# Performance work log

Measured on AMD Instinct MI355X. Metric: run time of the kernel, lower is better.

## Reference

```python
import jax, jax.numpy as jnp
import numpy as np

N_HEAD = 16
MA_K = 0.02          # sigmoid temperature in ma_k_activation
LEAKY_SLOPE = 0.02   # negative_slope in ma_q_activation
NEG_INF = -1e9


def setup_inputs() -> dict:
    key = jax.random.key(0)
    k1, k2, k3, k4 = jax.random.split(key, 4)
    B, T, C = 2, 2048, 1024
    x = jax.random.normal(k1, (B, T, C), dtype=jnp.float32)
    s = 1.0 / np.sqrt(C)
    W_attn = jax.random.normal(k2, (C, 2 * C), dtype=jnp.float32) * s
    W_k2 = jax.random.normal(k3, (C, C), dtype=jnp.float32) * s
    W_proj = jax.random.normal(k4, (C, C), dtype=jnp.float32) * s
    return {"x": x, "W_attn": W_attn, "W_k2": W_k2, "W_proj": W_proj}


def _heads(t, H):
    # [B,T,C] -> [B,H,T,d]
    B, T, C = t.shape
    return t.reshape(B, T, H, C // H).transpose(0, 2, 1, 3)


def reference(x, W_attn, W_k2, W_proj):
    B, T, C = x.shape
    H = N_HEAD
    d = C // H
    scale = 1.0 / jnp.sqrt(jnp.asarray(d, x.dtype))

    qk = x @ W_attn                      # [B,T,2C]
    q, k = jnp.split(qk, 2, axis=-1)
    q = _heads(q, H)                     # [B,H,T,d]
    k = _heads(k, H)
    v = _heads(x, H)                     # v = x

    # --- AR branch: causal softmax attention ---
    scores = jnp.einsum('bhtd,bhsd->bhts', q, k) * scale
    causal = jnp.tril(jnp.ones((T, T), dtype=bool))
    scores = jnp.where(causal, scores, NEG_INF)
    attn = jax.nn.softmax(scores, axis=-1)
    y = jnp.einsum('bhts,bhsd->bhtd', attn, v)   # [B,H,T,d]

    # --- MA branch: causal, softmax-free linear attention on residual ---
    e = v[:, :, 1:, :] - y[:, :, :-1, :]          # [B,H,T-1,d]
    k2 = _heads(x[:, :-1, :] @ W_k2, H)           # [B,H,T-1,d]
    q2 = q[:, :, 1:, :]                           # [B,H,T-1,d]

    qa = -jax.nn.leaky_relu(-q2 * scale, negative_slope=LEAKY_SLOPE)
    ka = jax.nn.sigmoid(MA_K * (k2 * scale))

    w = jnp.einsum('bhtd,bhsd->bhts', qa, ka)     # [B,H,T-1,T-1]
    w = jnp.tril(w)
    y2 = jnp.einsum('bhts,bhsd->bhtd', w, e)      # [B,H,T-1,d]
    y2 = jnp.concatenate([jnp.zeros_like(y2[:, :, :1, :]), y2], axis=2)  # pad front

    def merge(t):  # [B,H,T,d] -> [B,T,C]
        return t.transpose(0, 2, 1, 3).reshape(B, T, C)

    return merge(y) @ W_proj + merge(y2) @ W_proj
```

## Files before the change

kernel.cpp:

```cpp
#include <hip/hip_runtime.h>

typedef unsigned short u16;
typedef u16   u16x4  __attribute__((ext_vector_type(4)));
typedef u16   u16x8  __attribute__((ext_vector_type(8)));
typedef __bf16 bf16x8 __attribute__((ext_vector_type(8)));
typedef float  f32x4  __attribute__((ext_vector_type(4)));

__device__ __forceinline__ float bf2f(u16 v) {
    unsigned u = ((unsigned)v) << 16;
    return __builtin_bit_cast(float, u);
}
__device__ __forceinline__ u16 f2bf(float f) {
    unsigned u = __builtin_bit_cast(unsigned, f);
    u += 0x7fffu + ((u >> 16) & 1u);
    return (u16)(u >> 16);
}

__device__ __forceinline__ size_t kimg_idx(int bh, int s, int d) {
    return ((size_t)(bh * 32 + (s >> 6)) * 4096) + (size_t)(((d >> 3) * 64 + (s & 63)) * 8) + (d & 7);
}
__device__ __forceinline__ size_t vimg_idx(int bh, int s, int d) {
    return ((size_t)(bh * 32 + (s >> 6)) * 4096) + (size_t)((((s & 63) >> 3) * 64 + d) * 8) + (s & 7);
}

__global__ __launch_bounds__(256)
void convert_pack(const float* __restrict__ in, u16* __restrict__ xb,
                  u16* __restrict__ xpack) {
    int i = blockIdx.x * 256 + threadIdx.x;
    int c4 = i & 255, row = i >> 8;
    int s = row & 2047, b = row >> 11;
    float4 v = ((const float4*)in)[i];
    u16x4 o;
    o.x = f2bf(v.x); o.y = f2bf(v.y); o.z = f2bf(v.z); o.w = f2bf(v.w);
    ((u16x4*)xb)[i] = o;
    int h = c4 >> 4, d0 = (c4 & 15) * 4;
    size_t base = vimg_idx(b * 16 + h, s, d0);
    xpack[base]      = o.x;
    xpack[base + 8]  = o.y;
    xpack[base + 16] = o.z;
    xpack[base + 24] = o.w;
}

__global__ __launch_bounds__(256)
void prep_weights(const float* __restrict__ Wa, const float* __restrict__ Wk,
                  const float* __restrict__ Wp, u16* __restrict__ Wta,
                  u16* __restrict__ Wtk, u16* __restrict__ Wtp) {
    __shared__ u16 tile[64][65];
    const int bx = blockIdx.x;
    const float* in; u16* out; int Cd, cx;
    if (bx < 32)      { in = Wa; out = Wta; Cd = 2048; cx = bx; }
    else if (bx < 48) { in = Wk; out = Wtk; Cd = 1024; cx = bx - 32; }
    else              { in = Wp; out = Wtp; Cd = 1024; cx = bx - 48; }
    const int c0 = cx * 64, r0 = blockIdx.y * 64;
    const int tid = threadIdx.x;
#pragma unroll
    for (int i = 0; i < 16; ++i) {
        int idx = tid + i * 256;
        int r = idx >> 6, c = idx & 63;
        tile[r][c] = f2bf(in[(size_t)(r0 + r) * Cd + c0 + c]);
    }
    __syncthreads();
#pragma unroll
    for (int i = 0; i < 16; ++i) {
        int idx = tid + i * 256;
        int r = idx >> 6, c = idx & 63;
        out[(size_t)(c0 + r) * 1024 + r0 + c] = tile[c][r];
    }
}

__global__ __launch_bounds__(256, 2)
void gemm_qk(const u16* __restrict__ A, const u16* __restrict__ Bt,
             u16* __restrict__ qs, u16* __restrict__ kpack, int K) {
    __shared__ __align__(16) u16 As[4][128][8];
    __shared__ __align__(16) u16 Bs[4][128][8];
    const int tid = threadIdx.x;
    const int wave = tid >> 6, lane = tid & 63;
    const int m0 = blockIdx.y * 128, n0 = blockIdx.x * 128;
    const int wm = (wave >> 1) * 64, wn = (wave & 1) * 64;
    const int q = lane >> 4, mr = lane & 15;
    const int sr = tid >> 2, c8 = tid & 3;
    const u16* Ap = A + (size_t)(m0 + sr) * K + c8 * 8;
    const u16* Bp = Bt + (size_t)(n0 + sr) * K + c8 * 8;

    f32x4 acc[4][4];
#pragma unroll
    for (int i = 0; i < 4; ++i)
#pragma unroll
        for (int j = 0; j < 4; ++j) acc[i][j] = f32x4{0.f, 0.f, 0.f, 0.f};

    u16x8 a0, a1, b0, b1;
    auto gload = [&](int k0) {
        a0 = *(const u16x8*)(Ap + k0);
        a1 = *(const u16x8*)(Ap + k0 + (size_t)64 * K);
        b0 = *(const u16x8*)(Bp + k0);
        b1 = *(const u16x8*)(Bp + k0 + (size_t)64 * K);
    };
    gload(0);
    for (int k0 = 0; k0 < K; k0 += 32) {
        __syncthreads();
        *(u16x8*)&As[c8][sr][0]      = a0;
        *(u16x8*)&As[c8][sr + 64][0] = a1;
        *(u16x8*)&Bs[c8][sr][0]      = b0;
        *(u16x8*)&Bs[c8][sr + 64][0] = b1;
        __syncthreads();
        if (k0 + 32 < K) gload(k0 + 32);
        bf16x8 af[4], bfr[4];
#pragma unroll
        for (int i = 0; i < 4; ++i) af[i]  = *(const bf16x8*)&As[q][wm + i * 16 + mr][0];
#pragma unroll
        for (int j = 0; j < 4; ++j) bfr[j] = *(const bf16x8*)&Bs[q][wn + j * 16 + mr][0];
#pragma unroll
        for (int i = 0; i < 4; ++i)
#pragma unroll
            for (int j = 0; j < 4; ++j)
                acc[i][j] = __builtin_amdgcn_mfma_f32_16x16x32_bf16(af[i], bfr[j], acc[i][j], 0, 0, 0);
    }
#pragma unroll
    for (int i = 0; i < 4; ++i)
#pragma unroll
        for (int j = 0; j < 4; ++j)
#pragma unroll
            for (int r = 0; r < 4; ++r) {
                int m = m0 + wm + i * 16 + q * 4 + r;
                int n = n0 + wn + j * 16 + mr;
                float v = acc[i][j][r];
                if (n < 1024) {
                    qs[(size_t)m * 1024 + n] = f2bf(v * 0.125f);
                } else {
                    int b = m >> 11, s = m & 2047, nn = n - 1024;
                    kpack[kimg_idx(b * 16 + (nn >> 6), s, nn & 63)] = f2bf(v);
                }
            }
}

template <int EPI>
__global__ __launch_bounds__(256, 2)
void gemm64(const u16* __restrict__ A, const u16* __restrict__ Bt,
            void* __restrict__ Cv, int N, int K) {
    __shared__ __align__(16) u16 As[4][64][8];
    __shared__ __align__(16) u16 Bs[4][128][8];
    const int tid = threadIdx.x;
    const int wave = tid >> 6, lane = tid & 63;
    const int m0 = blockIdx.y * 64, n0 = blockIdx.x * 128;
    const int wn0 = wave * 32;
    const int q = lane >> 4, mr = lane & 15;
    const int sr = tid >> 2, c8 = tid & 3;
    const u16* Ap = A + (size_t)(m0 + sr) * K + c8 * 8;
    const u16* Bp = Bt + (size_t)(n0 + sr) * K + c8 * 8;

    f32x4 acc[4][2];
#pragma unroll
    for (int i = 0; i < 4; ++i)
#pragma unroll
        for (int j = 0; j < 2; ++j) acc[i][j] = f32x4{0.f, 0.f, 0.f, 0.f};

    u16x8 a0, b0, b1;
    auto gload = [&](int k0) {
        a0 = *(const u16x8*)(Ap + k0);
        b0 = *(const u16x8*)(Bp + k0);
        b1 = *(const u16x8*)(Bp + k0 + (size_t)64 * K);
    };
    gload(0);
    for (int k0 = 0; k0 < K; k0 += 32) {
        __syncthreads();
        *(u16x8*)&As[c8][sr][0]      = a0;
        *(u16x8*)&Bs[c8][sr][0]      = b0;
        *(u16x8*)&Bs[c8][sr + 64][0] = b1;
        __syncthreads();
        if (k0 + 32 < K) gload(k0 + 32);
        bf16x8 af[4], bfr[2];
#pragma unroll
        for (int i = 0; i < 4; ++i) af[i]  = *(const bf16x8*)&As[q][i * 16 + mr][0];
#pragma unroll
        for (int j = 0; j < 2; ++j) bfr[j] = *(const bf16x8*)&Bs[q][wn0 + j * 16 + mr][0];
#pragma unroll
        for (int i = 0; i < 4; ++i)
#pragma unroll
            for (int j = 0; j < 2; ++j)
                acc[i][j] = __builtin_amdgcn_mfma_f32_16x16x32_bf16(af[i], bfr[j], acc[i][j], 0, 0, 0);
    }
#pragma unroll
    for (int i = 0; i < 4; ++i)
#pragma unroll
        for (int j = 0; j < 2; ++j)
#pragma unroll
            for (int r = 0; r < 4; ++r) {
                int m = m0 + i * 16 + q * 4 + r;
                int n = n0 + wn0 + j * 16 + mr;
                float v = acc[i][j][r];
                if (EPI == 1) {
                    ((float*)Cv)[(size_t)m * N + n] = v;
                } else {
                    int b = m >> 11, s = m & 2047;
                    ((u16*)Cv)[kimg_idx(b * 16 + (n >> 6), s, n & 63)] =
                        f2bf(1.f / (1.f + __expf(-0.0025f * v)));
                }
            }
}

__global__ __launch_bounds__(256, 2)
void flash_mfma(const u16* __restrict__ qs, const u16* __restrict__ kpack,
                const u16* __restrict__ xpack, u16* __restrict__ Opart,
                float* __restrict__ lpart) {
    __shared__ __align__(16) u16 Ks[8][64][8];
    __shared__ __align__(16) u16 Vs[8][64][8];
    __shared__ __align__(16) u16 Ps[4][16][72];
    const int bh = blockIdx.y, b = bh >> 4, hc = (bh & 15) * 64;
    const int z = blockIdx.z;
    const int tid = threadIdx.x, w = tid >> 6, lane = tid & 63;
    const int n16 = lane & 15, quad = lane >> 4;
    const u16* kbase = kpack + (size_t)bh * 32 * 4096;
    const u16* vbase = xpack + (size_t)bh * 32 * 4096;
    u16* Ob = Opart + (size_t)z * 4096 * 1024;
    float* lb = lpart + z * 65536;

    for (int rep = 0; rep < 2; ++rep) {
        const int T = rep ? 15 - (int)blockIdx.x : (int)blockIdx.x;
        const int t0 = T * 128;
        const int nchunk = 2 * T + 2;

        bf16x8 qf[2][2];
#pragma unroll
        for (int mt = 0; mt < 2; ++mt) {
            const int trow = t0 + (w + mt * 4) * 16 + n16;
            const u16* qp = &qs[(size_t)(b * 2048 + trow) * 1024 + hc + quad * 8];
            qf[mt][0] = *(const bf16x8*)qp;
            qf[mt][1] = *(const bf16x8*)(qp + 32);
        }

        f32x4 O[2][4];
        float lsum[2][4];
#pragma unroll
        for (int mt = 0; mt < 2; ++mt)
#pragma unroll
            for (int jt = 0; jt < 4; ++jt) { O[mt][jt] = f32x4{0.f, 0.f, 0.f, 0.f}; }
#pragma unroll
        for (int mt = 0; mt < 2; ++mt)
#pragma unroll
            for (int r = 0; r < 4; ++r) lsum[mt][r] = 0.f;

        u16x8 kr0, kr1, vr0, vr1;
        auto pref = [&](int c) {
            const u16* kc = kbase + (size_t)c * 4096;
            const u16* vc = vbase + (size_t)c * 4096;
            kr0 = *(const u16x8*)(kc + tid * 8);
            kr1 = *(const u16x8*)(kc + (256 + tid) * 8);
            vr0 = *(const u16x8*)(vc + tid * 8);
            vr1 = *(const u16x8*)(vc + (256 + tid) * 8);
        };
        if (z < nchunk) pref(z);

        for (int c = z; c < nchunk; c += 2) {
            __syncthreads();
            *(u16x8*)((u16*)Ks + tid * 8)         = kr0;
            *(u16x8*)((u16*)Ks + (256 + tid) * 8) = kr1;
            *(u16x8*)((u16*)Vs + tid * 8)         = vr0;
            *(u16x8*)((u16*)Vs + (256 + tid) * 8) = vr1;
            __syncthreads();
            if (c + 2 < nchunk) pref(c + 2);

            f32x4 S[2][4];
#pragma unroll
            for (int mt = 0; mt < 2; ++mt)
#pragma unroll
                for (int jt = 0; jt < 4; ++jt) S[mt][jt] = f32x4{0.f, 0.f, 0.f, 0.f};
#pragma unroll
            for (int ks = 0; ks < 2; ++ks)
#pragma unroll
                for (int jt = 0; jt < 4; ++jt) {
                    bf16x8 kf = *(const bf16x8*)&Ks[ks * 4 + quad][jt * 16 + n16][0];
                    S[0][jt] = __builtin_amdgcn_mfma_f32_16x16x32_bf16(qf[0][ks], kf, S[0][jt], 0, 0, 0);
                    S[1][jt] = __builtin_amdgcn_mfma_f32_16x16x32_bf16(qf[1][ks], kf, S[1][jt], 0, 0, 0);
                }
            bf16x8 vf[2][4];
#pragma unroll
            for (int ks = 0; ks < 2; ++ks)
#pragma unroll
                for (int jt = 0; jt < 4; ++jt)
                    vf[ks][jt] = *(const bf16x8*)&Vs[ks * 4 + quad][jt * 16 + n16][0];

#pragma unroll
            for (int mt = 0; mt < 2; ++mt) {
                if (mt == 0 && c == 2 * T + 1) continue;
                float p[4][4];
#pragma unroll
                for (int reg = 0; reg < 4; ++reg)
#pragma unroll
                    for (int jt = 0; jt < 4; ++jt)
                        p[reg][jt] = __expf(S[mt][jt][reg]);
                if (c == 2 * T + mt) {
#pragma unroll
                    for (int reg = 0; reg < 4; ++reg) {
                        const int tr = t0 + (w + mt * 4) * 16 + quad * 4 + reg;
#pragma unroll
                        for (int jt = 0; jt < 4; ++jt)
                            if (c * 64 + jt * 16 + n16 > tr) p[reg][jt] = 0.f;
                    }
                }
#pragma unroll
                for (int reg = 0; reg < 4; ++reg) {
                    lsum[mt][reg] += (p[reg][0] + p[reg][1]) + (p[reg][2] + p[reg][3]);
#pragma unroll
                    for (int jt = 0; jt < 4; ++jt)
                        Ps[w][quad * 4 + reg][jt * 16 + n16] = f2bf(p[reg][jt]);
                }
                bf16x8 pf[2];
#pragma unroll
                for (int ks = 0; ks < 2; ++ks)
                    pf[ks] = *(const bf16x8*)&Ps[w][n16][ks * 32 + quad * 8];
#pragma unroll
                for (int ks = 0; ks < 2; ++ks)
#pragma unroll
                    for (int jt = 0; jt < 4; ++jt)
                        O[mt][jt] = __builtin_amdgcn_mfma_f32_16x16x32_bf16(pf[ks], vf[ks][jt], O[mt][jt], 0, 0, 0);
            }
        }

#pragma unroll
        for (int mt = 0; mt < 2; ++mt)
#pragma unroll
            for (int reg = 0; reg < 4; ++reg) {
                float l = lsum[mt][reg];
#pragma unroll
                for (int off = 1; off < 16; off <<= 1) l += __shfl_xor(l, off, 64);
                const int tr = t0 + (w + mt * 4) * 16 + quad * 4 + reg;
                if (n16 == 0) lb[bh * 2048 + tr] = l;
                const size_t row = (size_t)(b * 2048 + tr) * 1024 + hc;
#pragma unroll
                for (int jt = 0; jt < 4; ++jt)
                    Ob[row + jt * 16 + n16] = f2bf(O[mt][jt][reg]);
            }
    }
}

__global__ __launch_bounds__(256)
void combine_flash(const u16* __restrict__ Opart, const float* __restrict__ lpart,
                   const u16* __restrict__ xb, u16* __restrict__ y,
                   u16* __restrict__ epack) {
    int i = blockIdx.x * 256 + threadIdx.x;
    int c4 = i & 255, row = i >> 8, t = row & 2047, b = row >> 11;
    int h = c4 >> 4, d0 = (c4 & 15) * 4;
    size_t off = (size_t)row * 1024 + c4 * 4;
    u16x4 o0 = *(const u16x4*)&Opart[off];
    u16x4 o1 = *(const u16x4*)&Opart[(size_t)4096 * 1024 + off];
    int lrow = (b * 16 + h) * 2048 + t;
    float inv = 1.f / (lpart[lrow] + lpart[65536 + lrow]);
    float y0 = (bf2f(o0.x) + bf2f(o1.x)) * inv;
    float y1 = (bf2f(o0.y) + bf2f(o1.y)) * inv;
    float y2 = (bf2f(o0.z) + bf2f(o1.z)) * inv;
    float y3 = (bf2f(o0.w) + bf2f(o1.w)) * inv;
    u16x4 yo;
    yo.x = f2bf(y0); yo.y = f2bf(y1); yo.z = f2bf(y2); yo.w = f2bf(y3);
    *(u16x4*)&y[off] = yo;
    float e0 = 0.f, e1 = 0.f, e2 = 0.f, e3 = 0.f;
    if (t < 2047) {
        u16x4 xv = *(const u16x4*)&xb[off + 1024];
        e0 = bf2f(xv.x) - y0; e1 = bf2f(xv.y) - y1;
        e2 = bf2f(xv.z) - y2; e3 = bf2f(xv.w) - y3;
    }
    size_t base = vimg_idx(b * 16 + h, t, d0);
    epack[base]      = f2bf(e0);
    epack[base + 8]  = f2bf(e1);
    epack[base + 16] = f2bf(e2);
    epack[base + 24] = f2bf(e3);
}

__global__ __launch_bounds__(256, 2)
void arma_mfma(const u16* __restrict__ qs, const u16* __restrict__ kapack,
               const u16* __restrict__ epack, u16* __restrict__ Opart) {
    __shared__ __align__(16) u16 Ks[8][64][8];
    __shared__ __align__(16) u16 Es[8][64][8];
    __shared__ __align__(16) u16 Ps[4][16][72];
    const int bh = blockIdx.y, b = bh >> 4, hc = (bh & 15) * 64;
    const int z = blockIdx.z;
    const int tid = threadIdx.x, w = tid >> 6, lane = tid & 63;
    const int n16 = lane & 15, quad = lane >> 4;
    const u16* kbase = kapack + (size_t)bh * 32 * 4096;
    const u16* vbase = epack + (size_t)bh * 32 * 4096;
    u16* Ob = Opart + (size_t)z * 4096 * 1024;

    for (int rep = 0; rep < 2; ++rep) {
        const int T = rep ? 15 - (int)blockIdx.x : (int)blockIdx.x;
        const int t0 = T * 128;
        const int nchunk = 2 * T + 2;

        bf16x8 qf[2][2];
#pragma unroll
        for (int mt = 0; mt < 2; ++mt) {
            const int trow = t0 + (w + mt * 4) * 16 + n16;
            const u16* qp = &qs[(size_t)(b * 2048 + trow) * 1024 + hc + quad * 8];
#pragma unroll
            for (int ks = 0; ks < 2; ++ks) {
                u16x8 qv = *(const u16x8*)(qp + ks * 32);
                u16x8 o;
#pragma unroll
                for (int j = 0; j < 8; ++j) {
                    float zv = bf2f(qv[j]);
                    o[j] = f2bf(zv < 0.f ? zv : 0.02f * zv);
                }
                qf[mt][ks] = __builtin_bit_cast(bf16x8, o);
            }
        }

        f32x4 O[2][4];
#pragma unroll
        for (int mt = 0; mt < 2; ++mt)
#pragma unroll
            for (int jt = 0; jt < 4; ++jt) O[mt][jt] = f32x4{0.f, 0.f, 0.f, 0.f};

        u16x8 kr0, kr1, vr0, vr1;
        auto pref = [&](int c) {
            const u16* kc = kbase + (size_t)c * 4096;
            const u16* vc = vbase + (size_t)c * 4096;
            kr0 = *(const u16x8*)(kc + tid * 8);
            kr1 = *(const u16x8*)(kc + (256 + tid) * 8);
            vr0 = *(const u16x8*)(vc + tid * 8);
            vr1 = *(const u16x8*)(vc + (256 + tid) * 8);
        };
        if (z < nchunk) pref(z);

        for (int c = z; c < nchunk; c += 2) {
            __syncthreads();
            *(u16x8*)((u16*)Ks + tid * 8)         = kr0;
            *(u16x8*)((u16*)Ks + (256 + tid) * 8) = kr1;
            *(u16x8*)((u16*)Es + tid * 8)         = vr0;
            *(u16x8*)((u16*)Es + (256 + tid) * 8) = vr1;
            __syncthreads();
            if (c + 2 < nchunk) pref(c + 2);

            f32x4 S[2][4];
#pragma unroll
            for (int mt = 0; mt < 2; ++mt)
#pragma unroll
                for (int jt = 0; jt < 4; ++jt) S[mt][jt] = f32x4{0.f, 0.f, 0.f, 0.f};
#pragma unroll
            for (int ks = 0; ks < 2; ++ks)
#pragma unroll
                for (int jt = 0; jt < 4; ++jt) {
                    bf16x8 kf = *(const bf16x8*)&Ks[ks * 4 + quad][jt * 16 + n16][0];
                    S[0][jt] = __builtin_amdgcn_mfma_f32_16x16x32_bf16(qf[0][ks], kf, S[0][jt], 0, 0, 0);
                    S[1][jt] = __builtin_amdgcn_mfma_f32_16x16x32_bf16(qf[1][ks], kf, S[1][jt], 0, 0, 0);
                }
            bf16x8 vf[2][4];
#pragma unroll
            for (int ks = 0; ks < 2; ++ks)
#pragma unroll
                for (int jt = 0; jt < 4; ++jt)
                    vf[ks][jt] = *(const bf16x8*)&Es[ks * 4 + quad][jt * 16 + n16][0];

#pragma unroll
            for (int mt = 0; mt < 2; ++mt) {
                if (mt == 0 && c == 2 * T + 1) continue;
                if (c == 2 * T + mt) {
#pragma unroll
                    for (int reg = 0; reg < 4; ++reg) {
                        const int tr = t0 + (w + mt * 4) * 16 + quad * 4 + reg;
#pragma unroll
                        for (int jt = 0; jt < 4; ++jt)
                            if (c * 64 + jt * 16 + n16 >= tr) S[mt][jt][reg] = 0.f;
                    }
                }
#pragma unroll
                for (int reg = 0; reg < 4; ++reg)
#pragma unroll
                    for (int jt = 0; jt < 4; ++jt)
                        Ps[w][quad * 4 + reg][jt * 16 + n16] = f2bf(S[mt][jt][reg]);
                bf16x8 pf[2];
#pragma unroll
                for (int ks = 0; ks < 2; ++ks)
                    pf[ks] = *(const bf16x8*)&Ps[w][n16][ks * 32 + quad * 8];
#pragma unroll
                for (int ks = 0; ks < 2; ++ks)
#pragma unroll
                    for (int jt = 0; jt < 4; ++jt)
                        O[mt][jt] = __builtin_amdgcn_mfma_f32_16x16x32_bf16(pf[ks], vf[ks][jt], O[mt][jt], 0, 0, 0);
            }
        }

#pragma unroll
        for (int mt = 0; mt < 2; ++mt)
#pragma unroll
            for (int reg = 0; reg < 4; ++reg) {
                const int tr = t0 + (w + mt * 4) * 16 + quad * 4 + reg;
                const size_t row = (size_t)(b * 2048 + tr) * 1024 + hc;
#pragma unroll
                for (int jt = 0; jt < 4; ++jt)
                    Ob[row + jt * 16 + n16] = f2bf(O[mt][jt][reg]);
            }
    }
}

__global__ __launch_bounds__(256)
void combine_arma(const u16* __restrict__ Opart, const u16* __restrict__ y,
                  u16* __restrict__ ys) {
    int i = blockIdx.x * 256 + threadIdx.x;
    size_t off = (size_t)i * 4;
    u16x4 o0 = *(const u16x4*)&Opart[off];
    u16x4 o1 = *(const u16x4*)&Opart[(size_t)4096 * 1024 + off];
    u16x4 yv = *(const u16x4*)&y[off];
    u16x4 r;
    r.x = f2bf(bf2f(yv.x) + bf2f(o0.x) + bf2f(o1.x));
    r.y = f2bf(bf2f(yv.y) + bf2f(o0.y) + bf2f(o1.y));
    r.z = f2bf(bf2f(yv.z) + bf2f(o0.z) + bf2f(o1.z));
    r.w = f2bf(bf2f(yv.w) + bf2f(o0.w) + bf2f(o1.w));
    *(u16x4*)&ys[off] = r;
}

extern "C" void kernel_launch(void* const* d_in, const int* in_sizes, int n_in,
                              void* d_out, int out_size, void* d_ws, size_t ws_size,
                              hipStream_t stream) {
    const float* x      = (const float*)d_in[0];
    const float* W_attn = (const float*)d_in[1];
    const float* W_k2   = (const float*)d_in[2];
    const float* W_proj = (const float*)d_in[3];
    float* out = (float*)d_out;

    char* w = (char*)d_ws;
    u16* xb      = (u16*)w; w += (size_t)4096 * 1024 * 2;
    u16* Wt_attn = (u16*)w; w += (size_t)2048 * 1024 * 2;
    u16* Wt_k2   = (u16*)w; w += (size_t)1024 * 1024 * 2;
    u16* Wt_proj = (u16*)w; w += (size_t)1024 * 1024 * 2;
    u16* qs      = (u16*)w; w += (size_t)4096 * 1024 * 2;
    u16* kpack   = (u16*)w; w += (size_t)4096 * 1024 * 2;
    u16* kapack  = (u16*)w; w += (size_t)4096 * 1024 * 2;
    u16* xpack   = (u16*)w; w += (size_t)4096 * 1024 * 2;
    u16* y       = (u16*)w; w += (size_t)4096 * 1024 * 2;
    u16* epack   = (u16*)w; w += (size_t)4096 * 1024 * 2;
    u16* Opart   = (u16*)w; w += (size_t)2 * 4096 * 1024 * 2;
    float* lpart = (float*)w; w += (size_t)2 * 65536 * 4;
    u16* ys = xb;

    convert_pack<<<dim3(4096), dim3(256), 0, stream>>>(x, xb, xpack);
    prep_weights<<<dim3(64, 16), dim3(256), 0, stream>>>(W_attn, W_k2, W_proj,
                                                         Wt_attn, Wt_k2, Wt_proj);
    gemm_qk<<<dim3(16, 32), dim3(256), 0, stream>>>(xb, Wt_attn, qs, kpack, 1024);
    gemm64<2><<<dim3(8, 64), dim3(256), 0, stream>>>(xb, Wt_k2, kapack, 1024, 1024);
    flash_mfma<<<dim3(8, 32, 2), dim3(256), 0, stream>>>(qs, kpack, xpack, Opart, lpart);
    combine_flash<<<dim3(4096), dim3(256), 0, stream>>>(Opart, lpart, xb, y, epack);
    arma_mfma<<<dim3(8, 32, 2), dim3(256), 0, stream>>>(qs, kapack, epack, Opart);
    combine_arma<<<dim3(4096), dim3(256), 0, stream>>>(Opart, y, ys);
    gemm64<1><<<dim3(8, 64), dim3(256), 0, stream>>>(ys, Wt_proj, out, 1024, 1024);
}
```

Before: 281.9 us.

## Fuse QK and K2 projection GEMMs into one launch and swizzle LDS tiles

Merges the separate QK projection GEMM and the K2 projection GEMM into one kernel over a 24-column grid. This relies on Wt_k2 sitting directly after Wt_attn in the workspace, and applies the sigmoid epilogue for the third column range. Both GEMM kernels also get an XOR swizzle on LDS row indices to reduce bank conflicts, and the fused kernel raises its launch-bounds occupancy hint from 2 to 3. The aim is to cut one launch, fill the GPU with a larger grid, and reduce LDS conflicts. The cost is an implicit dependency on the workspace layout.

```diff
diff --git a/kernel.cpp b/kernel.cpp
--- a/kernel.cpp
+++ b/kernel.cpp
@@ -68,9 +68,11 @@
     }
 }
 
-__global__ __launch_bounds__(256, 2)
-void gemm_qk(const u16* __restrict__ A, const u16* __restrict__ Bt,
-             u16* __restrict__ qs, u16* __restrict__ kpack, int K) {
+__global__ __launch_bounds__(256, 3)
+void gemm_fused(const u16* __restrict__ A, const u16* __restrict__ Bt,
+                u16* __restrict__ qs, u16* __restrict__ kpack,
+                u16* __restrict__ kapack) {
+    const int K = 1024;
     __shared__ __align__(16) u16 As[4][128][8];
     __shared__ __align__(16) u16 Bs[4][128][8];
     const int tid = threadIdx.x;
@@ -79,6 +81,8 @@
     const int wm = (wave >> 1) * 64, wn = (wave & 1) * 64;
     const int q = lane >> 4, mr = lane & 15;
     const int sr = tid >> 2, c8 = tid & 3;
+    const int sw = c8 * 2;
+    const int rs = q * 2;
     const u16* Ap = A + (size_t)(m0 + sr) * K + c8 * 8;
     const u16* Bp = Bt + (size_t)(n0 + sr) * K + c8 * 8;
 
@@ -98,17 +102,17 @@
     gload(0);
     for (int k0 = 0; k0 < K; k0 += 32) {
         __syncthreads();
-        *(u16x8*)&As[c8][sr][0]      = a0;
-        *(u16x8*)&As[c8][sr + 64][0] = a1;
-        *(u16x8*)&Bs[c8][sr][0]      = b0;
-        *(u16x8*)&Bs[c8][sr + 64][0] = b1;
+        *(u16x8*)&As[c8][sr ^ sw][0]        = a0;
+        *(u16x8*)&As[c8][(sr + 64) ^ sw][0] = a1;
+        *(u16x8*)&Bs[c8][sr ^ sw][0]        = b0;
+        *(u16x8*)&Bs[c8][(sr + 64) ^ sw][0] = b1;
         __syncthreads();
         if (k0 + 32 < K) gload(k0 + 32);
         bf16x8 af[4], bfr[4];
 #pragma unroll
-        for (int i = 0; i < 4; ++i) af[i]  = *(const bf16x8*)&As[q][wm + i * 16 + mr][0];
-#pragma unroll
-        for (int j = 0; j < 4; ++j) bfr[j] = *(const bf16x8*)&Bs[q][wn + j * 16 + mr][0];
+        for (int i = 0; i < 4; ++i) af[i]  = *(const bf16x8*)&As[q][(wm + i * 16 + mr) ^ rs][0];
+#pragma unroll
+        for (int j = 0; j < 4; ++j) bfr[j] = *(const bf16x8*)&Bs[q][(wn + j * 16 + mr) ^ rs][0];
 #pragma unroll
         for (int i = 0; i < 4; ++i)
 #pragma unroll
@@ -124,19 +128,23 @@
                 int m = m0 + wm + i * 16 + q * 4 + r;
                 int n = n0 + wn + j * 16 + mr;
                 float v = acc[i][j][r];
+                int b = m >> 11, s = m & 2047;
                 if (n < 1024) {
                     qs[(size_t)m * 1024 + n] = f2bf(v * 0.125f);
+                } else if (n < 2048) {
+                    int nn = n - 1024;
+                    kpack[kimg_idx(b * 16 + (nn >> 6), s, nn & 63)] = f2bf(v);
                 } else {
-                    int b = m >> 11, s = m & 2047, nn = n - 1024;
-                    kpack[kimg_idx(b * 16 + (nn >> 6), s, nn & 63)] = f2bf(v);
-                }
-            }
-}
-
-template <int EPI>
+                    int nn = n - 2048;
+                    kapack[kimg_idx(b * 16 + (nn >> 6), s, nn & 63)] =
+                        f2bf(1.f / (1.f + __expf(-0.0025f * v)));
+                }
+            }
+}
+
 __global__ __launch_bounds__(256, 2)
 void gemm64(const u16* __restrict__ A, const u16* __restrict__ Bt,
-            void* __restrict__ Cv, int N, int K) {
+            float* __restrict__ Cv, int N, int K) {
     __shared__ __align__(16) u16 As[4][64][8];
     __shared__ __align__(16) u16 Bs[4][128][8];
     const int tid = threadIdx.x;
@@ -145,6 +153,7 @@
     const int wn0 = wave * 32;
     const int q = lane >> 4, mr = lane & 15;
     const int sr = tid >> 2, c8 = tid & 3;
+    const int sw = c8 * 2, rs = q * 2;
     const u16* Ap = A + (size_t)(m0 + sr) * K + c8 * 8;
     const u16* Bp = Bt + (size_t)(n0 + sr) * K + c8 * 8;
 
@@ -163,16 +172,17 @@
     gload(0);
     for (int k0 = 0; k0 < K; k0 += 32) {
         __syncthreads();
-        *(u16x8*)&As[c8][sr][0]      = a0;
-        *(u16x8*)&Bs[c8][sr][0]      = b0;
-        *(u16x8*)&Bs[c8][sr + 64][0] = b1;
+        if (sr < 64) *(u16x8*)&As[c8][sr ^ sw][0] = a0;
+        else         *(u16x8*)&As[c8][(sr - 64) ^ sw][0] = a0;
+        *(u16x8*)&Bs[c8][sr ^ sw][0]        = b0;
+        *(u16x8*)&Bs[c8][(sr + 64) ^ sw][0] = b1;
         __syncthreads();
         if (k0 + 32 < K) gload(k0 + 32);
         bf16x8 af[4], bfr[2];
 #pragma unroll
-        for (int i = 0; i < 4; ++i) af[i]  = *(const bf16x8*)&As[q][i * 16 + mr][0];
-#pragma unroll
-        for (int j = 0; j < 2; ++j) bfr[j] = *(const bf16x8*)&Bs[q][wn0 + j * 16 + mr][0];
+        for (int i = 0; i < 4; ++i) af[i]  = *(const bf16x8*)&As[q][(i * 16 + mr) ^ rs][0];
+#pragma unroll
+        for (int j = 0; j < 2; ++j) bfr[j] = *(const bf16x8*)&Bs[q][(wn0 + j * 16 + mr) ^ rs][0];
 #pragma unroll
         for (int i = 0; i < 4; ++i)
 #pragma unroll
@@ -187,14 +197,7 @@
             for (int r = 0; r < 4; ++r) {
                 int m = m0 + i * 16 + q * 4 + r;
                 int n = n0 + wn0 + j * 16 + mr;
-                float v = acc[i][j][r];
-                if (EPI == 1) {
-                    ((float*)Cv)[(size_t)m * N + n] = v;
-                } else {
-                    int b = m >> 11, s = m & 2047;
-                    ((u16*)Cv)[kimg_idx(b * 16 + (n >> 6), s, n & 63)] =
-                        f2bf(1.f / (1.f + __expf(-0.0025f * v)));
-                }
+                Cv[(size_t)m * N + n] = acc[i][j][r];
             }
 }
 
@@ -533,11 +536,10 @@
     convert_pack<<<dim3(4096), dim3(256), 0, stream>>>(x, xb, xpack);
     prep_weights<<<dim3(64, 16), dim3(256), 0, stream>>>(W_attn, W_k2, W_proj,
                                                          Wt_attn, Wt_k2, Wt_proj);
-    gemm_qk<<<dim3(16, 32), dim3(256), 0, stream>>>(xb, Wt_attn, qs, kpack, 1024);
-    gemm64<2><<<dim3(8, 64), dim3(256), 0, stream>>>(xb, Wt_k2, kapack, 1024, 1024);
+    gemm_fused<<<dim3(24, 32), dim3(256), 0, stream>>>(xb, Wt_attn, qs, kpack, kapack);
     flash_mfma<<<dim3(8, 32, 2), dim3(256), 0, stream>>>(qs, kpack, xpack, Opart, lpart);
     combine_flash<<<dim3(4096), dim3(256), 0, stream>>>(Opart, lpart, xb, y, epack);
     arma_mfma<<<dim3(8, 32, 2), dim3(256), 0, stream>>>(qs, kapack, epack, Opart);
     combine_arma<<<dim3(4096), dim3(256), 0, stream>>>(Opart, y, ys);
-    gemm64<1><<<dim3(8, 64), dim3(256), 0, stream>>>(ys, Wt_proj, out, 1024, 1024);
-}
+    gemm64<<<dim3(8, 64), dim3(256), 0, stream>>>(ys, Wt_proj, out, 1024, 1024);
+}
```

Measured after the change: 261.1 us. 7.4% less time.
